# Optimization experiments

Measured on AMD Instinct MI355X. Metric: run time of the kernel, lower is better.

## Reference

```python
import jax, jax.numpy as jnp
import numpy as np

N_NODES = 50000
N_EDGES = 800000
N_FEAT = 128
N_HIDDEN = 128
N_CLASSES = 64


def sage_mean_conv(x, src, dst, W_self, W_neigh, b, n_nodes):
    # DGL SAGEConv (mean): out = x @ W_self + mean_neigh(x) @ W_neigh + b
    # mean over in-neighbors: messages flow src -> dst
    msg = x[src]  # [E, F] gather
    h_sum = jax.ops.segment_sum(msg, dst, num_segments=n_nodes)  # [N, F]
    deg = jax.ops.segment_sum(jnp.ones((src.shape[0],), x.dtype), dst,
                              num_segments=n_nodes)
    h_mean = h_sum / jnp.maximum(deg, 1.0)[:, None]
    return x @ W_self + h_mean @ W_neigh + b


def setup_inputs() -> dict:
    key = jax.random.key(0)
    ks = jax.random.split(key, 8)
    sc1 = 1.0 / np.sqrt(N_FEAT)
    sc2 = 1.0 / np.sqrt(N_HIDDEN)
    return {
        "x": jax.random.normal(ks[0], (N_NODES, N_FEAT), jnp.float32),
        "W_self1": jax.random.normal(ks[1], (N_FEAT, N_HIDDEN), jnp.float32) * sc1,
        "W_neigh1": jax.random.normal(ks[2], (N_FEAT, N_HIDDEN), jnp.float32) * sc1,
        "b1": jnp.zeros((N_HIDDEN,), jnp.float32),
        "W_self2": jax.random.normal(ks[3], (N_HIDDEN, N_CLASSES), jnp.float32) * sc2,
        "W_neigh2": jax.random.normal(ks[4], (N_HIDDEN, N_CLASSES), jnp.float32) * sc2,
        "b2": jnp.zeros((N_CLASSES,), jnp.float32),
        "src": jax.random.randint(ks[5], (N_EDGES,), 0, N_NODES, jnp.int32),
        "dst": jax.random.randint(ks[6], (N_EDGES,), 0, N_NODES, jnp.int32),
    }


def reference(x, W_self1, W_neigh1, b1, W_self2, W_neigh2, b2, src, dst):
    n = x.shape[0]
    h = sage_mean_conv(x, src, dst, W_self1, W_neigh1, b1, n)
    h = jax.nn.relu(h)
    logits = sage_mean_conv(h, src, dst, W_self2, W_neigh2, b2, n)
    return logits
```

## Files before the change

kernel.cpp:

```cpp
#include <hip/hip_runtime.h>

#define N_NODES 50000
#define N_EDGES 800000
#define N_FEAT 128
#define N_HIDDEN 128
#define N_CLASSES 64

#define NBUCK 256
#define BUCK_NODES 196
#define BIN_CHUNK 8192
#define BIN_BLK ((N_EDGES + BIN_CHUNK - 1) / BIN_CHUNK)

#define CAST_BLK 6250
#define PACK1_BLK 16
#define PACK2_BLK 8
#define PREP_BLK (CAST_BLK + BIN_BLK + PACK1_BLK + PACK2_BLK)
#define GEMM1_BLK ((N_NODES + 31) / 32)
#define BG_BLK (BIN_BLK + GEMM1_BLK)

typedef __attribute__((ext_vector_type(8))) short bf16x8;
typedef __attribute__((ext_vector_type(4))) float f32x4;

__device__ __forceinline__ unsigned short f32_to_bf16(float f) {
    unsigned int u = __float_as_uint(f);
    return (unsigned short)((u + 0x7fffu + ((u >> 16) & 1u)) >> 16);
}
__device__ __forceinline__ float bf16lo(unsigned int v) { return __uint_as_float(v << 16); }
__device__ __forceinline__ float bf16hi(unsigned int v) { return __uint_as_float(v & 0xffff0000u); }

template <int NOUT>
__device__ void pack_w_body(int idx, const float* __restrict__ Wself,
                            const float* __restrict__ Wneigh,
                            unsigned short* __restrict__ Bp) {
    constexpr int NT = NOUT / 16;
    constexpr int NO = NOUT / 2;
    if (idx >= 4 * NT * 64) return;
    const int lane = idx & 63;
    const int tc = idx >> 6;
    const int c = tc % NT;
    const int t = tc / NT;
    const int n = c * 16 + (lane & 15);
    const int k0 = t * 32 + (lane >> 4) * 8;
    const float* W = (n < NO) ? Wself : Wneigh;
    const int nn = (n < NO) ? n : n - NO;
    ushort4 lo, hi;
    lo.x = f32_to_bf16(W[(k0 + 0) * NO + nn]);
    lo.y = f32_to_bf16(W[(k0 + 1) * NO + nn]);
    lo.z = f32_to_bf16(W[(k0 + 2) * NO + nn]);
    lo.w = f32_to_bf16(W[(k0 + 3) * NO + nn]);
    hi.x = f32_to_bf16(W[(k0 + 4) * NO + nn]);
    hi.y = f32_to_bf16(W[(k0 + 5) * NO + nn]);
    hi.z = f32_to_bf16(W[(k0 + 6) * NO + nn]);
    hi.w = f32_to_bf16(W[(k0 + 7) * NO + nn]);
    ((ushort4*)&Bp[(size_t)idx * 8])[0] = lo;
    ((ushort4*)&Bp[(size_t)idx * 8])[1] = hi;
}

__device__ void a0_body(int blk, const int* __restrict__ dst, int* __restrict__ bcount) {
    __shared__ int h[NBUCK];
    const int t = threadIdx.x;
    h[t] = 0;
    __syncthreads();
    const int lo = blk * BIN_CHUNK;
    const int hi = min(lo + BIN_CHUNK, N_EDGES);
    for (int i = lo + t; i < hi; i += 256) {
        atomicAdd(&h[dst[i] / BUCK_NODES], 1);
    }
    __syncthreads();
    if (h[t] > 0) atomicAdd(&bcount[t], h[t]);
}

__global__ __launch_bounds__(256) void prep_kernel(
        const float* __restrict__ x, unsigned short* __restrict__ xb,
        const int* __restrict__ dst, int* __restrict__ bcount,
        const float* __restrict__ Ws1, const float* __restrict__ Wn1,
        unsigned short* __restrict__ Bp1,
        const float* __restrict__ Ws2, const float* __restrict__ Wn2,
        unsigned short* __restrict__ Bp2) {
    const int b = blockIdx.x;
    const int t = threadIdx.x;
    if (b < CAST_BLK) {
        int i = b * 256 + t;
        float4 v = ((const float4*)x)[i];
        ushort4 o;
        o.x = f32_to_bf16(v.x);
        o.y = f32_to_bf16(v.y);
        o.z = f32_to_bf16(v.z);
        o.w = f32_to_bf16(v.w);
        ((ushort4*)xb)[i] = o;
    } else if (b < CAST_BLK + BIN_BLK) {
        a0_body(b - CAST_BLK, dst, bcount);
    } else if (b < CAST_BLK + BIN_BLK + PACK1_BLK) {
        int idx = (b - CAST_BLK - BIN_BLK) * 256 + t;
        pack_w_body<256>(idx, Ws1, Wn1, Bp1);
    } else {
        int idx = (b - CAST_BLK - BIN_BLK - PACK1_BLK) * 256 + t;
        pack_w_body<128>(idx, Ws2, Wn2, Bp2);
    }
}

__global__ __launch_bounds__(256) void bscan_kernel(const int* __restrict__ bcount,
                                                    int* __restrict__ bstart,
                                                    int* __restrict__ bcursor) {
    __shared__ int sc[NBUCK];
    const int t = threadIdx.x;
    const int v = bcount[t];
    sc[t] = v;
    __syncthreads();
    for (int s = 1; s < NBUCK; s <<= 1) {
        int u = (t >= s) ? sc[t - s] : 0;
        __syncthreads();
        sc[t] += u;
        __syncthreads();
    }
    const int excl = sc[t] - v;
    bstart[t] = excl;
    bcursor[t] = excl;
    if (t == NBUCK - 1) bstart[NBUCK] = sc[t];
}

__device__ void a1_body(int blk, const int* __restrict__ src, const int* __restrict__ dst,
                        int* __restrict__ bcursor, unsigned int* __restrict__ binned) {
    __shared__ int h[NBUCK];
    __shared__ int base[NBUCK];
    const int t = threadIdx.x;
    h[t] = 0;
    __syncthreads();
    const int lo = blk * BIN_CHUNK;
    const int hi = min(lo + BIN_CHUNK, N_EDGES);
    for (int i = lo + t; i < hi; i += 256) {
        atomicAdd(&h[dst[i] / BUCK_NODES], 1);
    }
    __syncthreads();
    if (h[t] > 0) base[t] = atomicAdd(&bcursor[t], h[t]);
    h[t] = 0;
    __syncthreads();
    for (int i = lo + t; i < hi; i += 256) {
        const int d = dst[i];
        const int b = d / BUCK_NODES;
        const int r = atomicAdd(&h[b], 1);
        binned[base[b] + r] = ((unsigned int)(d - b * BUCK_NODES) << 16) | (unsigned int)src[i];
    }
}

template <int NOUT>
__device__ void gemm_mfma_body(int gblk,
                               const unsigned short* __restrict__ xb,
                               const unsigned short* __restrict__ Bp,
                               const float* __restrict__ bias,
                               float* __restrict__ s,
                               unsigned short* __restrict__ p) {
    constexpr int NT = NOUT / 16;
    constexpr int NO = NOUT / 2;
    constexpr int NSUB = NT / 4;

    const int tid = threadIdx.x;
    const int wave = tid >> 6;
    const int lane = tid & 63;
    const int mcol = lane & 15;
    const int kgrp = lane >> 4;

    const int mbase = gblk * 32;
    int r0 = mbase + mcol;       if (r0 >= N_NODES) r0 = N_NODES - 1;
    int r1 = mbase + 16 + mcol;  if (r1 >= N_NODES) r1 = N_NODES - 1;

    f32x4 acc[2][NSUB];
#pragma unroll
    for (int mt = 0; mt < 2; ++mt)
#pragma unroll
        for (int c = 0; c < NSUB; ++c)
            acc[mt][c] = (f32x4){0.f, 0.f, 0.f, 0.f};

#pragma unroll
    for (int t = 0; t < 4; ++t) {
        bf16x8 a0 = *(const bf16x8*)&xb[(size_t)r0 * 128 + t * 32 + kgrp * 8];
        bf16x8 a1 = *(const bf16x8*)&xb[(size_t)r1 * 128 + t * 32 + kgrp * 8];
#pragma unroll
        for (int c = 0; c < NSUB; ++c) {
            const int ct = wave * NSUB + c;
            bf16x8 bfrag = *(const bf16x8*)&Bp[((size_t)(t * NT + ct) * 64 + lane) * 8];
            acc[0][c] = __builtin_amdgcn_mfma_f32_16x16x32_bf16(a0, bfrag, acc[0][c], 0, 0, 0);
            acc[1][c] = __builtin_amdgcn_mfma_f32_16x16x32_bf16(a1, bfrag, acc[1][c], 0, 0, 0);
        }
    }

    float bv[NSUB];
    int ncols[NSUB];
#pragma unroll
    for (int c = 0; c < NSUB; ++c) {
        ncols[c] = (wave * NSUB + c) * 16 + mcol;
        bv[c] = (ncols[c] < NO) ? bias[ncols[c]] : 0.f;
    }

#pragma unroll
    for (int mt = 0; mt < 2; ++mt) {
#pragma unroll
        for (int c = 0; c < NSUB; ++c) {
            const int ncol = ncols[c];
#pragma unroll
            for (int r = 0; r < 4; ++r) {
                const int node = mbase + mt * 16 + kgrp * 4 + r;
                if (node >= N_NODES) continue;
                const float v = acc[mt][c][r];
                if (ncol < NO) {
                    s[(size_t)node * NO + ncol] = v + bv[c];
                } else {
                    p[(size_t)node * NO + (ncol - NO)] = f32_to_bf16(v);
                }
            }
        }
    }
}

__global__ __launch_bounds__(256) void bin_gemm1_kernel(
        const int* __restrict__ src, const int* __restrict__ dst,
        int* __restrict__ bcursor, unsigned int* __restrict__ binned,
        const unsigned short* __restrict__ xb,
        const unsigned short* __restrict__ Bp1,
        const float* __restrict__ b1,
        float* __restrict__ s1, unsigned short* __restrict__ p1) {
    const int b = blockIdx.x;
    if (b < BIN_BLK) {
        a1_body(b, src, dst, bcursor, binned);
    } else {
        gemm_mfma_body<256>(b - BIN_BLK, xb, Bp1, b1, s1, p1);
    }
}

__global__ __launch_bounds__(256) void bucket_build_kernel(
        const unsigned int* __restrict__ binned,
        const int* __restrict__ bstart,
        int* __restrict__ offsets,
        unsigned short* __restrict__ csr16) {
    __shared__ int cnt[NBUCK];
    __shared__ int pre[NBUCK];
    const int b = blockIdx.x;
    const int t = threadIdx.x;
    const int n0 = b * BUCK_NODES;
    const int nn = min(N_NODES - n0, BUCK_NODES);
    const int e0 = bstart[b];
    const int e1 = bstart[b + 1];

    cnt[t] = 0;
    __syncthreads();
    for (int i = e0 + t; i < e1; i += 256) {
        atomicAdd(&cnt[binned[i] >> 16], 1);
    }
    __syncthreads();
    int v = cnt[t];
    pre[t] = v;
    __syncthreads();
    for (int s = 1; s < NBUCK; s <<= 1) {
        int u = (t >= s) ? pre[t - s] : 0;
        __syncthreads();
        pre[t] += u;
        __syncthreads();
    }
    const int excl = pre[t] - v;
    if (t < nn) offsets[n0 + t] = e0 + excl;
    if (b == 0 && t == 0) offsets[N_NODES] = N_EDGES;
    __syncthreads();
    pre[t] = excl;
    cnt[t] = 0;
    __syncthreads();
    for (int i = e0 + t; i < e1; i += 256) {
        const unsigned int u = binned[i];
        const int dl = (int)(u >> 16);
        const int r = atomicAdd(&cnt[dl], 1);
        csr16[e0 + pre[dl] + r] = (unsigned short)(u & 0xffffu);
    }
}

__global__ __launch_bounds__(256) void gemm2_kernel(
        const unsigned short* __restrict__ h1b,
        const unsigned short* __restrict__ Bp2,
        const float* __restrict__ b2,
        float* __restrict__ s2, unsigned short* __restrict__ p2) {
    gemm_mfma_body<128>(blockIdx.x, h1b, Bp2, b2, s2, p2);
}

__global__ __launch_bounds__(256) void agg_relu_128_kernel(
        const float* __restrict__ s,
        const unsigned short* __restrict__ p,
        const int* __restrict__ offsets,
        const unsigned short* __restrict__ csr16,
        unsigned short* __restrict__ h1b) {
    const int wave = threadIdx.x >> 6;
    const int lane = threadIdx.x & 63;
    const int half = lane >> 5;
    const int l = lane & 31;
    const int node = blockIdx.x * 4 + wave;
    if (node >= N_NODES) return;

    const int off0 = offsets[node];
    const int off1 = offsets[node + 1];
    const uint2* pp = (const uint2*)p;

    float a0 = 0.f, a1 = 0.f, a2 = 0.f, a3 = 0.f;
    int i = off0 + half;
    for (; i + 14 < off1; i += 16) {
        uint2 v0 = pp[(size_t)csr16[i + 0] * 32 + l];
        uint2 v1 = pp[(size_t)csr16[i + 2] * 32 + l];
        uint2 v2 = pp[(size_t)csr16[i + 4] * 32 + l];
        uint2 v3 = pp[(size_t)csr16[i + 6] * 32 + l];
        uint2 v4 = pp[(size_t)csr16[i + 8] * 32 + l];
        uint2 v5 = pp[(size_t)csr16[i + 10] * 32 + l];
        uint2 v6 = pp[(size_t)csr16[i + 12] * 32 + l];
        uint2 v7 = pp[(size_t)csr16[i + 14] * 32 + l];
        a0 += bf16lo(v0.x) + bf16lo(v1.x) + bf16lo(v2.x) + bf16lo(v3.x)
            + bf16lo(v4.x) + bf16lo(v5.x) + bf16lo(v6.x) + bf16lo(v7.x);
        a1 += bf16hi(v0.x) + bf16hi(v1.x) + bf16hi(v2.x) + bf16hi(v3.x)
            + bf16hi(v4.x) + bf16hi(v5.x) + bf16hi(v6.x) + bf16hi(v7.x);
        a2 += bf16lo(v0.y) + bf16lo(v1.y) + bf16lo(v2.y) + bf16lo(v3.y)
            + bf16lo(v4.y) + bf16lo(v5.y) + bf16lo(v6.y) + bf16lo(v7.y);
        a3 += bf16hi(v0.y) + bf16hi(v1.y) + bf16hi(v2.y) + bf16hi(v3.y)
            + bf16hi(v4.y) + bf16hi(v5.y) + bf16hi(v6.y) + bf16hi(v7.y);
    }
    for (; i < off1; i += 2) {
        uint2 v = pp[(size_t)csr16[i] * 32 + l];
        a0 += bf16lo(v.x);
        a1 += bf16hi(v.x);
        a2 += bf16lo(v.y);
        a3 += bf16hi(v.y);
    }
    a0 += __shfl_xor(a0, 32);
    a1 += __shfl_xor(a1, 32);
    a2 += __shfl_xor(a2, 32);
    a3 += __shfl_xor(a3, 32);

    if (half == 0) {
        const float invdeg = 1.0f / fmaxf((float)(off1 - off0), 1.0f);
        float4 sv = ((const float4*)s)[(size_t)node * 32 + l];
        ushort4 o;
        o.x = f32_to_bf16(fmaxf(sv.x + a0 * invdeg, 0.f));
        o.y = f32_to_bf16(fmaxf(sv.y + a1 * invdeg, 0.f));
        o.z = f32_to_bf16(fmaxf(sv.z + a2 * invdeg, 0.f));
        o.w = f32_to_bf16(fmaxf(sv.w + a3 * invdeg, 0.f));
        ((ushort4*)h1b)[(size_t)node * 32 + l] = o;
    }
}

__global__ __launch_bounds__(256) void agg_64_kernel(
        const unsigned short* __restrict__ p,
        const int* __restrict__ offsets,
        const unsigned short* __restrict__ csr16,
        float* __restrict__ out) {
    const int wave = threadIdx.x >> 6;
    const int lane = threadIdx.x & 63;
    const int q = lane >> 4;
    const int l = lane & 15;
    const int node = blockIdx.x * 4 + wave;
    if (node >= N_NODES) return;

    const int off0 = offsets[node];
    const int off1 = offsets[node + 1];
    const uint2* pp = (const uint2*)p;

    float a0 = 0.f, a1 = 0.f, a2 = 0.f, a3 = 0.f;
    int i = off0 + q;
    for (; i + 12 < off1; i += 16) {
        uint2 v0 = pp[(size_t)csr16[i + 0] * 16 + l];
        uint2 v1 = pp[(size_t)csr16[i + 4] * 16 + l];
        uint2 v2 = pp[(size_t)csr16[i + 8] * 16 + l];
        uint2 v3 = pp[(size_t)csr16[i + 12] * 16 + l];
        a0 += bf16lo(v0.x) + bf16lo(v1.x) + bf16lo(v2.x) + bf16lo(v3.x);
        a1 += bf16hi(v0.x) + bf16hi(v1.x) + bf16hi(v2.x) + bf16hi(v3.x);
        a2 += bf16lo(v0.y) + bf16lo(v1.y) + bf16lo(v2.y) + bf16lo(v3.y);
        a3 += bf16hi(v0.y) + bf16hi(v1.y) + bf16hi(v2.y) + bf16hi(v3.y);
    }
    for (; i < off1; i += 4) {
        uint2 v = pp[(size_t)csr16[i] * 16 + l];
        a0 += bf16lo(v.x);
        a1 += bf16hi(v.x);
        a2 += bf16lo(v.y);
        a3 += bf16hi(v.y);
    }
    a0 += __shfl_xor(a0, 16); a0 += __shfl_xor(a0, 32);
    a1 += __shfl_xor(a1, 16); a1 += __shfl_xor(a1, 32);
    a2 += __shfl_xor(a2, 16); a2 += __shfl_xor(a2, 32);
    a3 += __shfl_xor(a3, 16); a3 += __shfl_xor(a3, 32);

    if (q == 0) {
        const float invdeg = 1.0f / fmaxf((float)(off1 - off0), 1.0f);
        float4 sv = ((float4*)out)[(size_t)node * 16 + l];
        sv.x += a0 * invdeg;
        sv.y += a1 * invdeg;
        sv.z += a2 * invdeg;
        sv.w += a3 * invdeg;
        ((float4*)out)[(size_t)node * 16 + l] = sv;
    }
}

extern "C" void kernel_launch(void* const* d_in, const int* in_sizes, int n_in,
                              void* d_out, int out_size, void* d_ws, size_t ws_size,
                              hipStream_t stream) {
    const float* x        = (const float*)d_in[0];
    const float* W_self1  = (const float*)d_in[1];
    const float* W_neigh1 = (const float*)d_in[2];
    const float* b1       = (const float*)d_in[3];
    const float* W_self2  = (const float*)d_in[4];
    const float* W_neigh2 = (const float*)d_in[5];
    const float* b2       = (const float*)d_in[6];
    const int*   src      = (const int*)d_in[7];
    const int*   dst      = (const int*)d_in[8];
    float* out = (float*)d_out;

    int* bcount  = (int*)d_ws;
    int* bstart  = bcount + 256;
    int* bcursor = bstart + 288;
    int* offsets = bcursor + 256;
    unsigned int* binned = (unsigned int*)(offsets + 50048);
    unsigned short* csr16 = (unsigned short*)(binned + 800000);
    unsigned short* Bp1 = csr16 + 800000;
    unsigned short* Bp2 = Bp1 + 32768;
    unsigned short* xb  = Bp2 + 16384;
    unsigned short* h1b = xb;
    float* s1 = (float*)(xb + (size_t)N_NODES * 128);
    unsigned short* p1 = (unsigned short*)(s1 + (size_t)N_NODES * 128);
    unsigned short* p2 = p1;

    hipMemsetAsync(bcount, 0, 256 * sizeof(int), stream);
    prep_kernel<<<PREP_BLK, 256, 0, stream>>>(x, xb, dst, bcount,
                                              W_self1, W_neigh1, Bp1,
                                              W_self2, W_neigh2, Bp2);

    bscan_kernel<<<1, 256, 0, stream>>>(bcount, bstart, bcursor);

    bin_gemm1_kernel<<<BG_BLK, 256, 0, stream>>>(src, dst, bcursor, binned,
                                                 xb, Bp1, b1, s1, p1);

    bucket_build_kernel<<<NBUCK, 256, 0, stream>>>(binned, bstart, offsets, csr16);

    agg_relu_128_kernel<<<(N_NODES + 3) / 4, 256, 0, stream>>>(s1, p1, offsets, csr16, h1b);

    gemm2_kernel<<<(N_NODES + 31) / 32, 256, 0, stream>>>(h1b, Bp2, b2, out, p2);
    agg_64_kernel<<<(N_NODES + 3) / 4, 256, 0, stream>>>(p2, offsets, csr16, out);
}
```

Baseline: 232.0 us.

## Widen aggregation gathers to 16-byte loads and shrink binning chunk size

Both aggregation kernels now gather neighbor rows with uint4 (16-byte) loads instead of uint2. Each lane therefore covers 8 bf16 features, and more neighbors are processed in parallel per wave: 4 edge streams for the 128-wide layer and 8 for the 64-wide layer. Reductions use an extra shuffle level. Separately, the binning chunk in bin_gemm1 shrinks to 2048 edges, giving more blocks, while the histogram pass keeps its own 8192 chunk. The goal is fewer memory instructions per gathered byte and more edge-level parallelism, at the cost of extra shuffles and more atomic traffic on the bucket cursors.

Result: faster. 209.7 us (-9.6%).

```diff
diff --git a/kernel.cpp b/kernel.cpp
--- a/kernel.cpp
+++ b/kernel.cpp
@@ -8,13 +8,15 @@
 
 #define NBUCK 256
 #define BUCK_NODES 196
-#define BIN_CHUNK 8192
+#define A0_CHUNK 8192
+#define A0_BLK ((N_EDGES + A0_CHUNK - 1) / A0_CHUNK)
+#define BIN_CHUNK 2048
 #define BIN_BLK ((N_EDGES + BIN_CHUNK - 1) / BIN_CHUNK)
 
 #define CAST_BLK 6250
 #define PACK1_BLK 16
 #define PACK2_BLK 8
-#define PREP_BLK (CAST_BLK + BIN_BLK + PACK1_BLK + PACK2_BLK)
+#define PREP_BLK (CAST_BLK + A0_BLK + PACK1_BLK + PACK2_BLK)
 #define GEMM1_BLK ((N_NODES + 31) / 32)
 #define BG_BLK (BIN_BLK + GEMM1_BLK)
 
@@ -61,8 +63,8 @@
     const int t = threadIdx.x;
     h[t] = 0;
     __syncthreads();
-    const int lo = blk * BIN_CHUNK;
-    const int hi = min(lo + BIN_CHUNK, N_EDGES);
+    const int lo = blk * A0_CHUNK;
+    const int hi = min(lo + A0_CHUNK, N_EDGES);
     for (int i = lo + t; i < hi; i += 256) {
         atomicAdd(&h[dst[i] / BUCK_NODES], 1);
     }
@@ -88,13 +90,13 @@
         o.z = f32_to_bf16(v.z);
         o.w = f32_to_bf16(v.w);
         ((ushort4*)xb)[i] = o;
-    } else if (b < CAST_BLK + BIN_BLK) {
+    } else if (b < CAST_BLK + A0_BLK) {
         a0_body(b - CAST_BLK, dst, bcount);
-    } else if (b < CAST_BLK + BIN_BLK + PACK1_BLK) {
-        int idx = (b - CAST_BLK - BIN_BLK) * 256 + t;
+    } else if (b < CAST_BLK + A0_BLK + PACK1_BLK) {
+        int idx = (b - CAST_BLK - A0_BLK) * 256 + t;
         pack_w_body<256>(idx, Ws1, Wn1, Bp1);
     } else {
-        int idx = (b - CAST_BLK - BIN_BLK - PACK1_BLK) * 256 + t;
+        int idx = (b - CAST_BLK - A0_BLK - PACK1_BLK) * 256 + t;
         pack_w_body<128>(idx, Ws2, Wn2, Bp2);
     }
 }
@@ -287,56 +289,63 @@
         unsigned short* __restrict__ h1b) {
     const int wave = threadIdx.x >> 6;
     const int lane = threadIdx.x & 63;
-    const int half = lane >> 5;
-    const int l = lane & 31;
+    const int q = lane >> 4;
+    const int l = lane & 15;
     const int node = blockIdx.x * 4 + wave;
     if (node >= N_NODES) return;
 
     const int off0 = offsets[node];
     const int off1 = offsets[node + 1];
-    const uint2* pp = (const uint2*)p;
+    const uint4* pp = (const uint4*)p;
 
     float a0 = 0.f, a1 = 0.f, a2 = 0.f, a3 = 0.f;
-    int i = off0 + half;
-    for (; i + 14 < off1; i += 16) {
-        uint2 v0 = pp[(size_t)csr16[i + 0] * 32 + l];
-        uint2 v1 = pp[(size_t)csr16[i + 2] * 32 + l];
-        uint2 v2 = pp[(size_t)csr16[i + 4] * 32 + l];
-        uint2 v3 = pp[(size_t)csr16[i + 6] * 32 + l];
-        uint2 v4 = pp[(size_t)csr16[i + 8] * 32 + l];
-        uint2 v5 = pp[(size_t)csr16[i + 10] * 32 + l];
-        uint2 v6 = pp[(size_t)csr16[i + 12] * 32 + l];
-        uint2 v7 = pp[(size_t)csr16[i + 14] * 32 + l];
-        a0 += bf16lo(v0.x) + bf16lo(v1.x) + bf16lo(v2.x) + bf16lo(v3.x)
-            + bf16lo(v4.x) + bf16lo(v5.x) + bf16lo(v6.x) + bf16lo(v7.x);
-        a1 += bf16hi(v0.x) + bf16hi(v1.x) + bf16hi(v2.x) + bf16hi(v3.x)
-            + bf16hi(v4.x) + bf16hi(v5.x) + bf16hi(v6.x) + bf16hi(v7.x);
-        a2 += bf16lo(v0.y) + bf16lo(v1.y) + bf16lo(v2.y) + bf16lo(v3.y)
-            + bf16lo(v4.y) + bf16lo(v5.y) + bf16lo(v6.y) + bf16lo(v7.y);
-        a3 += bf16hi(v0.y) + bf16hi(v1.y) + bf16hi(v2.y) + bf16hi(v3.y)
-            + bf16hi(v4.y) + bf16hi(v5.y) + bf16hi(v6.y) + bf16hi(v7.y);
-    }
-    for (; i < off1; i += 2) {
-        uint2 v = pp[(size_t)csr16[i] * 32 + l];
-        a0 += bf16lo(v.x);
-        a1 += bf16hi(v.x);
-        a2 += bf16lo(v.y);
-        a3 += bf16hi(v.y);
-    }
-    a0 += __shfl_xor(a0, 32);
-    a1 += __shfl_xor(a1, 32);
-    a2 += __shfl_xor(a2, 32);
-    a3 += __shfl_xor(a3, 32);
-
-    if (half == 0) {
+    float a4 = 0.f, a5 = 0.f, a6 = 0.f, a7 = 0.f;
+    int i = off0 + q;
+    for (; i + 12 < off1; i += 16) {
+        uint4 v0 = pp[(size_t)csr16[i + 0] * 16 + l];
+        uint4 v1 = pp[(size_t)csr16[i + 4] * 16 + l];
+        uint4 v2 = pp[(size_t)csr16[i + 8] * 16 + l];
+        uint4 v3 = pp[(size_t)csr16[i + 12] * 16 + l];
+        a0 += bf16lo(v0.x) + bf16lo(v1.x) + bf16lo(v2.x) + bf16lo(v3.x);
+        a1 += bf16hi(v0.x) + bf16hi(v1.x) + bf16hi(v2.x) + bf16hi(v3.x);
+        a2 += bf16lo(v0.y) + bf16lo(v1.y) + bf16lo(v2.y) + bf16lo(v3.y);
+        a3 += bf16hi(v0.y) + bf16hi(v1.y) + bf16hi(v2.y) + bf16hi(v3.y);
+        a4 += bf16lo(v0.z) + bf16lo(v1.z) + bf16lo(v2.z) + bf16lo(v3.z);
+        a5 += bf16hi(v0.z) + bf16hi(v1.z) + bf16hi(v2.z) + bf16hi(v3.z);
+        a6 += bf16lo(v0.w) + bf16lo(v1.w) + bf16lo(v2.w) + bf16lo(v3.w);
+        a7 += bf16hi(v0.w) + bf16hi(v1.w) + bf16hi(v2.w) + bf16hi(v3.w);
+    }
+    for (; i < off1; i += 4) {
+        uint4 v = pp[(size_t)csr16[i] * 16 + l];
+        a0 += bf16lo(v.x); a1 += bf16hi(v.x);
+        a2 += bf16lo(v.y); a3 += bf16hi(v.y);
+        a4 += bf16lo(v.z); a5 += bf16hi(v.z);
+        a6 += bf16lo(v.w); a7 += bf16hi(v.w);
+    }
+    a0 += __shfl_xor(a0, 16); a0 += __shfl_xor(a0, 32);
+    a1 += __shfl_xor(a1, 16); a1 += __shfl_xor(a1, 32);
+    a2 += __shfl_xor(a2, 16); a2 += __shfl_xor(a2, 32);
+    a3 += __shfl_xor(a3, 16); a3 += __shfl_xor(a3, 32);
+    a4 += __shfl_xor(a4, 16); a4 += __shfl_xor(a4, 32);
+    a5 += __shfl_xor(a5, 16); a5 += __shfl_xor(a5, 32);
+    a6 += __shfl_xor(a6, 16); a6 += __shfl_xor(a6, 32);
+    a7 += __shfl_xor(a7, 16); a7 += __shfl_xor(a7, 32);
+
+    if (q == 0) {
         const float invdeg = 1.0f / fmaxf((float)(off1 - off0), 1.0f);
-        float4 sv = ((const float4*)s)[(size_t)node * 32 + l];
-        ushort4 o;
-        o.x = f32_to_bf16(fmaxf(sv.x + a0 * invdeg, 0.f));
-        o.y = f32_to_bf16(fmaxf(sv.y + a1 * invdeg, 0.f));
-        o.z = f32_to_bf16(fmaxf(sv.z + a2 * invdeg, 0.f));
-        o.w = f32_to_bf16(fmaxf(sv.w + a3 * invdeg, 0.f));
-        ((ushort4*)h1b)[(size_t)node * 32 + l] = o;
+        float4 s0 = ((const float4*)s)[(size_t)node * 32 + l * 2];
+        float4 s1 = ((const float4*)s)[(size_t)node * 32 + l * 2 + 1];
+        ushort4 o0, o1;
+        o0.x = f32_to_bf16(fmaxf(s0.x + a0 * invdeg, 0.f));
+        o0.y = f32_to_bf16(fmaxf(s0.y + a1 * invdeg, 0.f));
+        o0.z = f32_to_bf16(fmaxf(s0.z + a2 * invdeg, 0.f));
+        o0.w = f32_to_bf16(fmaxf(s0.w + a3 * invdeg, 0.f));
+        o1.x = f32_to_bf16(fmaxf(s1.x + a4 * invdeg, 0.f));
+        o1.y = f32_to_bf16(fmaxf(s1.y + a5 * invdeg, 0.f));
+        o1.z = f32_to_bf16(fmaxf(s1.z + a6 * invdeg, 0.f));
+        o1.w = f32_to_bf16(fmaxf(s1.w + a7 * invdeg, 0.f));
+        ((ushort4*)h1b)[(size_t)node * 32 + l * 2] = o0;
+        ((ushort4*)h1b)[(size_t)node * 32 + l * 2 + 1] = o1;
     }
 }
 
@@ -347,47 +356,58 @@
         float* __restrict__ out) {
     const int wave = threadIdx.x >> 6;
     const int lane = threadIdx.x & 63;
-    const int q = lane >> 4;
-    const int l = lane & 15;
+    const int st = lane >> 3;
+    const int l = lane & 7;
     const int node = blockIdx.x * 4 + wave;
     if (node >= N_NODES) return;
 
     const int off0 = offsets[node];
     const int off1 = offsets[node + 1];
-    const uint2* pp = (const uint2*)p;
+    const uint4* pp = (const uint4*)p;
 
     float a0 = 0.f, a1 = 0.f, a2 = 0.f, a3 = 0.f;
-    int i = off0 + q;
-    for (; i + 12 < off1; i += 16) {
-        uint2 v0 = pp[(size_t)csr16[i + 0] * 16 + l];
-        uint2 v1 = pp[(size_t)csr16[i + 4] * 16 + l];
-        uint2 v2 = pp[(size_t)csr16[i + 8] * 16 + l];
-        uint2 v3 = pp[(size_t)csr16[i + 12] * 16 + l];
+    float a4 = 0.f, a5 = 0.f, a6 = 0.f, a7 = 0.f;
+    int i = off0 + st;
+    for (; i + 24 < off1; i += 32) {
+        uint4 v0 = pp[(size_t)csr16[i + 0] * 8 + l];
+        uint4 v1 = pp[(size_t)csr16[i + 8] * 8 + l];
+        uint4 v2 = pp[(size_t)csr16[i + 16] * 8 + l];
+        uint4 v3 = pp[(size_t)csr16[i + 24] * 8 + l];
         a0 += bf16lo(v0.x) + bf16lo(v1.x) + bf16lo(v2.x) + bf16lo(v3.x);
         a1 += bf16hi(v0.x) + bf16hi(v1.x) + bf16hi(v2.x) + bf16hi(v3.x);
         a2 += bf16lo(v0.y) + bf16lo(v1.y) + bf16lo(v2.y) + bf16lo(v3.y);
         a3 += bf16hi(v0.y) + bf16hi(v1.y) + bf16hi(v2.y) + bf16hi(v3.y);
-    }
-    for (; i < off1; i += 4) {
-        uint2 v = pp[(size_t)csr16[i] * 16 + l];
-        a0 += bf16lo(v.x);
-        a1 += bf16hi(v.x);
-        a2 += bf16lo(v.y);
-        a3 += bf16hi(v.y);
-    }
-    a0 += __shfl_xor(a0, 16); a0 += __shfl_xor(a0, 32);
-    a1 += __shfl_xor(a1, 16); a1 += __shfl_xor(a1, 32);
-    a2 += __shfl_xor(a2, 16); a2 += __shfl_xor(a2, 32);
-    a3 += __shfl_xor(a3, 16); a3 += __shfl_xor(a3, 32);
-
-    if (q == 0) {
+        a4 += bf16lo(v0.z) + bf16lo(v1.z) + bf16lo(v2.z) + bf16lo(v3.z);
+        a5 += bf16hi(v0.z) + bf16hi(v1.z) + bf16hi(v2.z) + bf16hi(v3.z);
+        a6 += bf16lo(v0.w) + bf16lo(v1.w) + bf16lo(v2.w) + bf16lo(v3.w);
+        a7 += bf16hi(v0.w) + bf16hi(v1.w) + bf16hi(v2.w) + bf16hi(v3.w);
+    }
+    for (; i < off1; i += 8) {
+        uint4 v = pp[(size_t)csr16[i] * 8 + l];
+        a0 += bf16lo(v.x); a1 += bf16hi(v.x);
+        a2 += bf16lo(v.y); a3 += bf16hi(v.y);
+        a4 += bf16lo(v.z); a5 += bf16hi(v.z);
+        a6 += bf16lo(v.w); a7 += bf16hi(v.w);
+    }
+    a0 += __shfl_xor(a0, 8); a0 += __shfl_xor(a0, 16); a0 += __shfl_xor(a0, 32);
+    a1 += __shfl_xor(a1, 8); a1 += __shfl_xor(a1, 16); a1 += __shfl_xor(a1, 32);
+    a2 += __shfl_xor(a2, 8); a2 += __shfl_xor(a2, 16); a2 += __shfl_xor(a2, 32);
+    a3 += __shfl_xor(a3, 8); a3 += __shfl_xor(a3, 16); a3 += __shfl_xor(a3, 32);
+    a4 += __shfl_xor(a4, 8); a4 += __shfl_xor(a4, 16); a4 += __shfl_xor(a4, 32);
+    a5 += __shfl_xor(a5, 8); a5 += __shfl_xor(a5, 16); a5 += __shfl_xor(a5, 32);
+    a6 += __shfl_xor(a6, 8); a6 += __shfl_xor(a6, 16); a6 += __shfl_xor(a6, 32);
+    a7 += __shfl_xor(a7, 8); a7 += __shfl_xor(a7, 16); a7 += __shfl_xor(a7, 32);
+
+    if (st == 0) {
         const float invdeg = 1.0f / fmaxf((float)(off1 - off0), 1.0f);
-        float4 sv = ((float4*)out)[(size_t)node * 16 + l];
-        sv.x += a0 * invdeg;
-        sv.y += a1 * invdeg;
-        sv.z += a2 * invdeg;
-        sv.w += a3 * invdeg;
-        ((float4*)out)[(size_t)node * 16 + l] = sv;
+        float4 s0 = ((float4*)out)[(size_t)node * 16 + l * 2];
+        float4 s1 = ((float4*)out)[(size_t)node * 16 + l * 2 + 1];
+        s0.x += a0 * invdeg; s0.y += a1 * invdeg;
+        s0.z += a2 * invdeg; s0.w += a3 * invdeg;
+        s1.x += a4 * invdeg; s1.y += a5 * invdeg;
+        s1.z += a6 * invdeg; s1.w += a7 * invdeg;
+        ((float4*)out)[(size_t)node * 16 + l * 2] = s0;
+        ((float4*)out)[(size_t)node * 16 + l * 2 + 1] = s1;
     }
 }
 
@@ -423,16 +443,11 @@
     prep_kernel<<<PREP_BLK, 256, 0, stream>>>(x, xb, dst, bcount,
                                               W_self1, W_neigh1, Bp1,
                                               W_self2, W_neigh2, Bp2);
-
     bscan_kernel<<<1, 256, 0, stream>>>(bcount, bstart, bcursor);
-
     bin_gemm1_kernel<<<BG_BLK, 256, 0, stream>>>(src, dst, bcursor, binned,
                                                  xb, Bp1, b1, s1, p1);
-
     bucket_build_kernel<<<NBUCK, 256, 0, stream>>>(binned, bstart, offsets, csr16);
-
     agg_relu_128_kernel<<<(N_NODES + 3) / 4, 256, 0, stream>>>(s1, p1, offsets, csr16, h1b);
-
     gemm2_kernel<<<(N_NODES + 31) / 32, 256, 0, stream>>>(h1b, Bp2, b2, out, p2);
     agg_64_kernel<<<(N_NODES + 3) / 4, 256, 0, stream>>>(p2, offsets, csr16, out);
 }
```
